# Optimization experiments

Measured on AMD Instinct MI355X. Metric: run time of the kernel, lower is better.

## Reference

```python
import math
import jax, jax.numpy as jnp
import numpy as np

B, S, D, H, DK = 2, 2048, 1024, 16, 64
NUM_BUCKETS, MAX_DISTANCE = 32, 128


def _relative_position_bucket(rel_pos):
    # bidirectional=True (encoder): is_decoder=False
    nb = NUM_BUCKETS // 2
    rel_buckets = (rel_pos > 0).astype(jnp.int32) * nb
    rp = jnp.abs(rel_pos)
    max_exact = nb // 2
    is_small = rp < max_exact
    rp_large = max_exact + (
        jnp.log(rp.astype(jnp.float32) / max_exact)
        / math.log(MAX_DISTANCE / max_exact)
        * (nb - max_exact)
    ).astype(jnp.int32)
    rp_large = jnp.minimum(rp_large, nb - 1)
    return rel_buckets + jnp.where(is_small, rp, rp_large)


def compute_bias(rel_bias, q_len, k_len):
    ctx = jnp.arange(q_len, dtype=jnp.int32)[:, None]
    mem = jnp.arange(k_len, dtype=jnp.int32)[None, :]
    buckets = _relative_position_bucket(mem - ctx)          # [q,k]
    vals = rel_bias[buckets]                                 # [q,k,H]
    return jnp.transpose(vals, (2, 0, 1))[None]              # [1,H,q,k]


def setup_inputs() -> dict:
    key = jax.random.key(0)
    ks = jax.random.split(key, 6)
    scale = 0.02
    return {
        "hidden_states": jax.random.normal(ks[0], (B, S, D), jnp.float32),
        "Wq": jax.random.normal(ks[1], (D, H * DK), jnp.float32) * scale,
        "Wk": jax.random.normal(ks[2], (D, H * DK), jnp.float32) * scale,
        "Wv": jax.random.normal(ks[3], (D, H * DK), jnp.float32) * scale,
        "Wo": jax.random.normal(ks[4], (H * DK, D), jnp.float32) * scale,
        "rel_bias": jax.random.normal(ks[5], (NUM_BUCKETS, H), jnp.float32) * scale,
    }


def reference(hidden_states, Wq, Wk, Wv, Wo, rel_bias):
    b, s, _ = hidden_states.shape

    def shape(x):  # [b,s,H*DK] -> [b,H,s,DK]
        return x.reshape(b, s, H, DK).transpose(0, 2, 1, 3)

    q = shape(hidden_states @ Wq)
    k = shape(hidden_states @ Wk)
    v = shape(hidden_states @ Wv)

    # T5: no 1/sqrt(d_k) scaling
    scores = jnp.einsum("bhqd,bhkd->bhqk", q, k)
    position_bias = compute_bias(rel_bias, s, s)             # [1,H,s,s]
    scores = scores + position_bias
    attn = jax.nn.softmax(scores.astype(jnp.float32), axis=-1).astype(scores.dtype)
    out = jnp.einsum("bhqk,bhkd->bhqd", attn, v)
    out = out.transpose(0, 2, 1, 3).reshape(b, s, H * DK)
    return out @ Wo
```

## Files before the change

kernel.cpp:

```cpp
#include <hip/hip_runtime.h>

#define HH 16
#define DKK 64
#define SS 2048
#define BB 2
#define DD 1024

typedef __attribute__((ext_vector_type(4))) float f32x4;
typedef __attribute__((ext_vector_type(16))) float f32x16;
typedef __attribute__((ext_vector_type(8))) short bf16x8;
typedef __attribute__((ext_vector_type(4))) short s16x4;
typedef __attribute__((ext_vector_type(4))) int i32x4;

#define WAITCNT_VM0 0xF70

__device__ __forceinline__ short bf16b(float f) {
    union { float f; unsigned u; } x; x.f = f;
    unsigned r = (x.u + 0x7fffu + ((x.u >> 16) & 1u)) >> 16;
    return (short)r;
}

__device__ __forceinline__ f32x4 mfma16(bf16x8 a, bf16x8 b, f32x4 c) {
    return __builtin_amdgcn_mfma_f32_16x16x32_bf16(a, b, c, 0, 0, 0);
}

__device__ __forceinline__ f32x16 mfma32(bf16x8 a, bf16x8 b, f32x16 c) {
    return __builtin_amdgcn_mfma_f32_32x32x16_bf16(a, b, c, 0, 0, 0);
}

__device__ __forceinline__ void lds16(const short* g, short* l) {
    __builtin_amdgcn_global_load_lds(
        (const __attribute__((address_space(1))) void*)g,
        (__attribute__((address_space(3))) void*)l, 16, 0, 0);
}

__device__ __forceinline__ int cvtpk(float lo, float hi) {
    int r;
    asm("v_cvt_pk_bf16_f32 %0, %1, %2" : "=v"(r) : "v"(lo), "v"(hi));
    return r;
}

__device__ __forceinline__ void swap32(int& a, int& b) {
    asm("v_permlane32_swap_b32 %0, %1" : "+v"(a), "+v"(b));
}

__global__ __launch_bounds__(256) void prep(
    const float* __restrict__ hs,
    const float* __restrict__ W0, const float* __restrict__ W1,
    const float* __restrict__ W2, const float* __restrict__ W3,
    const float* __restrict__ rb,
    short* __restrict__ hsb,
    short* __restrict__ T0, short* __restrict__ T1,
    short* __restrict__ T2, short* __restrict__ T3,
    float* __restrict__ tab) {
    __shared__ short tile[32][33];
    int blk = blockIdx.x, tid = threadIdx.x;
    if (blk < 4096) {
        int i = (blk * 256 + tid) * 4;
        f32x4 v = *(const f32x4*)(hs + i);
        s16x4 o;
        o.x = bf16b(v.x); o.y = bf16b(v.y); o.z = bf16b(v.z); o.w = bf16b(v.w);
        *(s16x4*)(hsb + i) = o;
    } else if (blk < 8192) {
        int t = blk - 4096;
        int z = t >> 10, r = t & 1023;
        int bx = r & 31, by = r >> 5;
        const float* W; short* T;
        switch (z) {
            case 0: W = W0; T = T0; break;
            case 1: W = W1; T = T1; break;
            case 2: W = W2; T = T2; break;
            default: W = W3; T = T3; break;
        }
        int n0 = bx * 32, k0 = by * 32;
        int tx = tid & 31, ty = (tid >> 5) * 4;
#pragma unroll
        for (int i = 0; i < 4; i++)
            tile[ty + i][tx] = bf16b(W[(k0 + ty + i) * DD + n0 + tx]);
        __syncthreads();
#pragma unroll
        for (int i = 0; i < 4; i++)
            T[(n0 + ty + i) * DD + k0 + tx] = tile[tx][ty + i];
    } else {
        int idx = (blk - 8192) * 256 + tid;
        if (idx < HH * 4095) {
            int h = idx / 4095, d = idx % 4095;
            int rel = d - 2047;
            int bucket = (rel > 0) ? 16 : 0;
            unsigned rr = (rel < 0) ? (unsigned)(-rel) : (unsigned)rel;
            int add;
            if (rr < 8) add = (int)rr;
            else {
                int e = 31 - __clz(rr);
                unsigned long long r2 = (unsigned long long)rr * (unsigned long long)rr;
                int f = 2 * e + ((r2 >= (2ull << (2 * e))) ? 1 : 0);
                add = 8 + (f - 6);
                if (add > 15) add = 15;
            }
            bucket += add;
            tab[h * 4095 + d] = rb[bucket * HH + h] * 1.44269504f;
        }
    }
}

__global__ __launch_bounds__(256) void gemm_qkv(
    const short* __restrict__ A, const short* __restrict__ Wt,
    short* __restrict__ Cq, short* __restrict__ Ck, short* __restrict__ Cvt) {
    const int K = 1024;
    __shared__ short As[128 * 64];
    __shared__ short Bs[128 * 64];
    int tid = threadIdx.x;
    int wave = tid >> 6, lane = tid & 63;
    int quad = lane >> 4, l16 = lane & 15;
    int m0 = blockIdx.y * 128, n0 = blockIdx.x * 128;

    int wm = (wave & 1) * 64, wn = (wave >> 1) * 64;
    int r0 = tid >> 3;
    int c0 = ((tid & 7) ^ (r0 & 7)) * 8;
    int ex7 = l16 & 7;

    f32x4 acc[4][4];
#pragma unroll
    for (int i = 0; i < 4; i++)
#pragma unroll
        for (int j = 0; j < 4; j++) acc[i][j] = (f32x4){0.f, 0.f, 0.f, 0.f};

    for (int k0 = 0; k0 < K; k0 += 64) {
        __syncthreads();
#pragma unroll
        for (int j = 0; j < 4; j++) {
            lds16(A + (size_t)(m0 + j * 32 + r0) * K + k0 + c0,
                  As + j * 2048 + wave * 512);
            lds16(Wt + (size_t)(n0 + j * 32 + r0) * K + k0 + c0,
                  Bs + j * 2048 + wave * 512);
        }
        __syncthreads();
#pragma unroll
        for (int kh = 0; kh < 2; kh++) {
            bf16x8 af[4], bfr[4];
#pragma unroll
            for (int t = 0; t < 4; t++) {
                int sl = (((kh * 4 + quad) ^ ex7)) * 8;
                af[t] = *(const bf16x8*)(As + (wm + t * 16 + l16) * 64 + sl);
                bfr[t] = *(const bf16x8*)(Bs + (wn + t * 16 + l16) * 64 + sl);
            }
#pragma unroll
            for (int mt = 0; mt < 4; mt++)
#pragma unroll
                for (int nt = 0; nt < 4; nt++)
                    acc[mt][nt] = mfma16(af[mt], bfr[nt], acc[mt][nt]);
        }
    }

#pragma unroll
    for (int mt = 0; mt < 4; mt++) {
#pragma unroll
        for (int nt = 0; nt < 4; nt++) {
#pragma unroll
            for (int r = 0; r < 4; r++) {
                int gm = m0 + wm + mt * 16 + quad * 4 + r;
                int gn = n0 + wn + nt * 16 + l16;
                int b = gm >> 11, s = gm & 2047;
                int which = gn >> 10;
                int h = (gn >> 6) & 15, dk = gn & 63;
                short bv = bf16b(acc[mt][nt][r]);
                if (which == 0)
                    Cq[(((size_t)(b * HH + h)) * SS + s) * DKK + dk] = bv;
                else if (which == 1)
                    Ck[(((size_t)(b * HH + h)) * SS + s) * DKK + dk] = bv;
                else
                    Cvt[(((size_t)(b * HH + h)) * DKK + dk) * SS + s] = bv;
            }
        }
    }
}

__global__ __launch_bounds__(256) void gemm_out(
    const short* __restrict__ A, const short* __restrict__ Wt,
    float* __restrict__ Cout) {
    const int K = 1024, N = 1024;
    __shared__ short As[64 * 64];
    __shared__ short Bs[128 * 64];
    int tid = threadIdx.x;
    int wave = tid >> 6, lane = tid & 63;
    int quad = lane >> 4, l16 = lane & 15;
    int m0 = blockIdx.y * 64, n0 = blockIdx.x * 128;

    int wm = (wave & 1) * 32, wn = (wave >> 1) * 64;
    int r0 = tid >> 3;
    int c0 = ((tid & 7) ^ (r0 & 7)) * 8;
    int ex7 = l16 & 7;

    f32x4 acc[2][4];
#pragma unroll
    for (int i = 0; i < 2; i++)
#pragma unroll
        for (int j = 0; j < 4; j++) acc[i][j] = (f32x4){0.f, 0.f, 0.f, 0.f};

    for (int k0 = 0; k0 < K; k0 += 64) {
        __syncthreads();
#pragma unroll
        for (int j = 0; j < 2; j++)
            lds16(A + (size_t)(m0 + j * 32 + r0) * K + k0 + c0,
                  As + j * 2048 + wave * 512);
#pragma unroll
        for (int j = 0; j < 4; j++)
            lds16(Wt + (size_t)(n0 + j * 32 + r0) * K + k0 + c0,
                  Bs + j * 2048 + wave * 512);
        __syncthreads();
#pragma unroll
        for (int kh = 0; kh < 2; kh++) {
            bf16x8 af[2], bfr[4];
            int sl = (((kh * 4 + quad) ^ ex7)) * 8;
#pragma unroll
            for (int t = 0; t < 2; t++)
                af[t] = *(const bf16x8*)(As + (wm + t * 16 + l16) * 64 + sl);
#pragma unroll
            for (int t = 0; t < 4; t++)
                bfr[t] = *(const bf16x8*)(Bs + (wn + t * 16 + l16) * 64 + sl);
#pragma unroll
            for (int mt = 0; mt < 2; mt++)
#pragma unroll
                for (int nt = 0; nt < 4; nt++)
                    acc[mt][nt] = mfma16(af[mt], bfr[nt], acc[mt][nt]);
        }
    }

#pragma unroll
    for (int mt = 0; mt < 2; mt++)
#pragma unroll
        for (int nt = 0; nt < 4; nt++)
#pragma unroll
            for (int r = 0; r < 4; r++) {
                int gm = m0 + wm + mt * 16 + quad * 4 + r;
                int gn = n0 + wn + nt * 16 + l16;
                Cout[(size_t)gm * N + gn] = acc[mt][nt][r];
            }
}

__global__ __launch_bounds__(256, 2) void attn(
    const short* __restrict__ Q, const short* __restrict__ Kmat,
    const short* __restrict__ Vt, const float* __restrict__ btab,
    short* __restrict__ O) {
    __shared__ short Ks[2][64 * 64];
    __shared__ short Vs[2][64 * 64];
    __shared__ float Linv[4][32];

    int tid = threadIdx.x;
    int wave = tid >> 6, lane = tid & 63;
    int el = lane & 31, hi = lane >> 5;
    int ex7 = el & 7;
    int bh = blockIdx.x;
    int h = bh & 15, b = bh >> 4;
    int q0b = blockIdx.y * 128;
    int q0w = q0b + wave * 32;

    const short* Qb = Q + (size_t)bh * SS * DKK;
    const short* Kb = Kmat + (size_t)bh * SS * DKK;
    const short* Vb = Vt + (size_t)bh * DKK * SS;
    const float* bt = btab + h * 4095;

    float blo = bt[2047 - 128];
    float bhi = bt[2047 + 128];

    int kro = tid >> 3;
    int gk = (tid & 7) ^ (kro & 7);
    const short* Kg0 = Kb + (size_t)kro * DKK + gk * 8;
    const short* Kg1 = Kb + (size_t)(kro + 32) * DKK + gk * 8;
    const short* Vg0 = Vb + (size_t)kro * SS + gk * 8;
    const short* Vg1 = Vb + (size_t)(kro + 32) * SS + gk * 8;

    bf16x8 qB[4];
#pragma unroll
    for (int c = 0; c < 4; c++)
        qB[c] = *(const bf16x8*)(Qb + (size_t)(q0w + el) * DKK + c * 16 + hi * 8);

    f32x16 o0, o1;
#pragma unroll
    for (int i = 0; i < 16; i++) { o0[i] = 0.f; o1[i] = 0.f; }
    float ls0 = 0.f, ls1 = 0.f, ls2 = 0.f, ls3 = 0.f;

    int bq = 2047 - q0w - el;

    lds16(Kg0, &Ks[0][wave * 512]);
    lds16(Kg1, &Ks[0][2048 + wave * 512]);
    lds16(Vg0, &Vs[0][wave * 512]);
    lds16(Vg1, &Vs[0][2048 + wave * 512]);

    int cur = 0;
    for (int kc = 0; kc < SS; kc += 64) {
        __syncthreads();
        int kn = (kc + 64) & (SS - 1);
        int nxt = cur ^ 1;
        lds16(Kg0 + (size_t)kn * DKK, &Ks[nxt][wave * 512]);
        lds16(Kg1 + (size_t)kn * DKK, &Ks[nxt][2048 + wave * 512]);
        lds16(Vg0 + kn, &Vs[nxt][wave * 512]);
        lds16(Vg1 + kn, &Vs[nxt][2048 + wave * 512]);

        const short* Ksc = &Ks[cur][0];
        const short* Vsc = &Vs[cur][0];

        bf16x8 vf[4][2];
#pragma unroll
        for (int c4 = 0; c4 < 4; c4++)
#pragma unroll
            for (int m = 0; m < 2; m++)
                vf[c4][m] = *(const bf16x8*)(
                    Vsc + (m * 32 + el) * 64 + (((2 * c4 + hi) ^ ex7) * 8));

#pragma unroll
        for (int st = 0; st < 2; st++) {
            f32x16 acc;
#pragma unroll
            for (int i = 0; i < 16; i++) acc[i] = 0.f;
#pragma unroll
            for (int c = 0; c < 4; c++) {
                bf16x8 kA = *(const bf16x8*)(
                    Ksc + (st * 32 + el) * 64 + (((2 * c + hi) ^ ex7) * 8));
                acc = mfma32(kA, qB[c], acc);
            }

            int ks = kc + st * 32;
            float br[16];
            if (ks > q0w - 159 && ks < q0w + 159) {
#pragma unroll
                for (int r = 0; r < 16; r++)
                    br[r] = bt[bq + ks + ((r & 3) + 8 * (r >> 2) + 4 * hi)];
            } else {
                float bc = (ks <= q0w - 159) ? blo : bhi;
#pragma unroll
                for (int r = 0; r < 16; r++) br[r] = bc;
            }

            float p[16];
#pragma unroll
            for (int r = 0; r < 16; r++)
                p[r] = __builtin_amdgcn_exp2f(
                    fmaf(acc[r], 1.44269504f, br[r]));
#pragma unroll
            for (int r = 0; r < 16; r += 4) {
                ls0 += p[r]; ls1 += p[r + 1]; ls2 += p[r + 2]; ls3 += p[r + 3];
            }

            int A1 = cvtpk(p[0], p[1]),   A2 = cvtpk(p[2], p[3]);
            int B1 = cvtpk(p[4], p[5]),   B2 = cvtpk(p[6], p[7]);
            int C1 = cvtpk(p[8], p[9]),   C2 = cvtpk(p[10], p[11]);
            int D1 = cvtpk(p[12], p[13]), D2 = cvtpk(p[14], p[15]);
            swap32(A1, B1); swap32(A2, B2);
            swap32(C1, D1); swap32(C2, D2);
            bf16x8 pf0 = __builtin_bit_cast(bf16x8, (i32x4){A1, A2, B1, B2});
            bf16x8 pf1 = __builtin_bit_cast(bf16x8, (i32x4){C1, C2, D1, D2});

            o0 = mfma32(pf0, vf[st * 2 + 0][0], o0);
            o1 = mfma32(pf0, vf[st * 2 + 0][1], o1);
            o0 = mfma32(pf1, vf[st * 2 + 1][0], o0);
            o1 = mfma32(pf1, vf[st * 2 + 1][1], o1);
        }
        cur ^= 1;
    }
    __builtin_amdgcn_s_waitcnt(WAITCNT_VM0);

    float lsum = (ls0 + ls1) + (ls2 + ls3);
    float tot = lsum + __shfl_xor(lsum, 32);
    float inv = 1.f / tot;
    if (hi == 0) Linv[wave][el] = inv;
    __asm__ __volatile__("" ::: "memory");

#pragma unroll
    for (int r = 0; r < 16; r++) {
        int qm = (r & 3) + 8 * (r >> 2) + 4 * hi;
        float iv = Linv[wave][qm];
        size_t base = ((size_t)(b * SS + q0w + qm)) * (HH * DKK) + h * DKK;
        O[base + el] = bf16b(o0[r] * iv);
        O[base + 32 + el] = bf16b(o1[r] * iv);
    }
}

extern "C" void kernel_launch(void* const* d_in, const int* in_sizes, int n_in,
                              void* d_out, int out_size, void* d_ws, size_t ws_size,
                              hipStream_t stream) {
    const float* hs = (const float*)d_in[0];
    const float* Wq = (const float*)d_in[1];
    const float* Wk = (const float*)d_in[2];
    const float* Wv = (const float*)d_in[3];
    const float* Wo = (const float*)d_in[4];
    const float* rb = (const float*)d_in[5];
    float* out = (float*)d_out;

    char* ws = (char*)d_ws;
    size_t off = 0;
    auto alloc = [&](size_t bytes) -> void* {
        void* p = (void*)(ws + off);
        off += (bytes + 255) & ~(size_t)255;
        return p;
    };
    const size_t M = (size_t)BB * SS;
    short* hsb = (short*)alloc(M * DD * 2);
    short* WqT = (short*)alloc((size_t)DD * DD * 2);
    short* WkT = (short*)alloc((size_t)DD * DD * 2);
    short* WvT = (short*)alloc((size_t)DD * DD * 2);
    short* WoT = (short*)alloc((size_t)DD * DD * 2);
    short* Qb  = (short*)alloc(M * DD * 2);
    short* Kb  = (short*)alloc(M * DD * 2);
    short* VTb = (short*)alloc(M * DD * 2);
    short* Ab  = (short*)alloc(M * DD * 2);
    float* btab = (float*)alloc((size_t)HH * 4095 * 4);

    prep<<<8448, 256, 0, stream>>>(hs, Wq, Wk, Wv, Wo, rb,
                                   hsb, WqT, WkT, WvT, WoT, btab);
    gemm_qkv<<<dim3(24, 32), 256, 0, stream>>>(hsb, WqT, Qb, Kb, VTb);
    attn<<<dim3(32, 16), 256, 0, stream>>>(Qb, Kb, VTb, btab, Ab);
    gemm_out<<<dim3(8, 64), 256, 0, stream>>>(Ab, WoT, out);
}
```

Measured before the change: 190.3 us.

## Fuse four kernels into one persistent megakernel with grid-wide barriers

Replaces the prep, QKV GEMM, attention and output GEMM launches with a single persistent kernel of 768 blocks. The phases are separated by atomic-counter grid barriers, and shared memory is unioned across phases. The aim is to remove inter-kernel launch gaps and tail effects. The costs are spin-wait barriers, only 512 of 768 blocks working in the attention and output phases, a launch bound of 3 blocks per CU that may limit registers, and reliance on every block being co-resident.

```diff
diff --git a/kernel.cpp b/kernel.cpp
--- a/kernel.cpp
+++ b/kernel.cpp
@@ -5,6 +5,7 @@
 #define SS 2048
 #define BB 2
 #define DD 1024
+#define NBLK 768
 
 typedef __attribute__((ext_vector_type(4))) float f32x4;
 typedef __attribute__((ext_vector_type(16))) float f32x16;
@@ -44,7 +45,20 @@
     asm("v_permlane32_swap_b32 %0, %1" : "+v"(a), "+v"(b));
 }
 
-__global__ __launch_bounds__(256) void prep(
+__device__ __forceinline__ void gsync(unsigned* bar, unsigned target) {
+    __syncthreads();
+    if (threadIdx.x == 0) {
+        __threadfence();
+        __hip_atomic_fetch_add(bar, 1u, __ATOMIC_ACQ_REL,
+                               __HIP_MEMORY_SCOPE_AGENT);
+        while (__hip_atomic_load(bar, __ATOMIC_ACQUIRE,
+                                 __HIP_MEMORY_SCOPE_AGENT) < target)
+            __builtin_amdgcn_s_sleep(4);
+    }
+    __syncthreads();
+}
+
+__global__ __launch_bounds__(256, 3) void mega(
     const float* __restrict__ hs,
     const float* __restrict__ W0, const float* __restrict__ W1,
     const float* __restrict__ W2, const float* __restrict__ W3,
@@ -52,327 +66,331 @@
     short* __restrict__ hsb,
     short* __restrict__ T0, short* __restrict__ T1,
     short* __restrict__ T2, short* __restrict__ T3,
-    float* __restrict__ tab) {
-    __shared__ short tile[32][33];
-    int blk = blockIdx.x, tid = threadIdx.x;
-    if (blk < 4096) {
-        int i = (blk * 256 + tid) * 4;
-        f32x4 v = *(const f32x4*)(hs + i);
-        s16x4 o;
-        o.x = bf16b(v.x); o.y = bf16b(v.y); o.z = bf16b(v.z); o.w = bf16b(v.w);
-        *(s16x4*)(hsb + i) = o;
-    } else if (blk < 8192) {
-        int t = blk - 4096;
-        int z = t >> 10, r = t & 1023;
-        int bx = r & 31, by = r >> 5;
-        const float* W; short* T;
-        switch (z) {
-            case 0: W = W0; T = T0; break;
-            case 1: W = W1; T = T1; break;
-            case 2: W = W2; T = T2; break;
-            default: W = W3; T = T3; break;
-        }
-        int n0 = bx * 32, k0 = by * 32;
-        int tx = tid & 31, ty = (tid >> 5) * 4;
+    float* __restrict__ tab,
+    short* __restrict__ Qb_, short* __restrict__ Kb_, short* __restrict__ VTb,
+    short* __restrict__ Ab, float* __restrict__ out,
+    unsigned* __restrict__ bars) {
+    __shared__ union {
+        short tile[32][33];
+        struct { short As[128 * 64]; short Bs[128 * 64]; } g;
+        struct { short Ks[2][4096]; short Vs[2][4096];
+                 float Linv[4][32]; } a;
+        struct { short As[64 * 64]; short Bs[128 * 64]; } o;
+    } sm;
+
+    int bid = blockIdx.x, tid = threadIdx.x;
+
+    for (int u = 0; u < 11; u++) {
+        int blk = bid + u * NBLK;
+        if (blk < 4096) {
+            int i = (blk * 256 + tid) * 4;
+            f32x4 v = *(const f32x4*)(hs + i);
+            s16x4 o;
+            o.x = bf16b(v.x); o.y = bf16b(v.y); o.z = bf16b(v.z); o.w = bf16b(v.w);
+            *(s16x4*)(hsb + i) = o;
+        } else if (blk < 8192) {
+            int t = blk - 4096;
+            int z = t >> 10, r = t & 1023;
+            int bx = r & 31, by = r >> 5;
+            const float* W; short* T;
+            switch (z) {
+                case 0: W = W0; T = T0; break;
+                case 1: W = W1; T = T1; break;
+                case 2: W = W2; T = T2; break;
+                default: W = W3; T = T3; break;
+            }
+            int n0 = bx * 32, k0 = by * 32;
+            int tx = tid & 31, ty = (tid >> 5) * 4;
+#pragma unroll
+            for (int i = 0; i < 4; i++)
+                sm.tile[ty + i][tx] = bf16b(W[(k0 + ty + i) * DD + n0 + tx]);
+            __syncthreads();
+#pragma unroll
+            for (int i = 0; i < 4; i++)
+                T[(n0 + ty + i) * DD + k0 + tx] = sm.tile[tx][ty + i];
+        } else {
+            int idx = (blk - 8192) * 256 + tid;
+            if (idx < HH * 4095) {
+                int h = idx / 4095, d = idx % 4095;
+                int rel = d - 2047;
+                int bucket = (rel > 0) ? 16 : 0;
+                unsigned rr = (rel < 0) ? (unsigned)(-rel) : (unsigned)rel;
+                int add;
+                if (rr < 8) add = (int)rr;
+                else {
+                    int e = 31 - __clz(rr);
+                    unsigned long long r2 =
+                        (unsigned long long)rr * (unsigned long long)rr;
+                    int f = 2 * e + ((r2 >= (2ull << (2 * e))) ? 1 : 0);
+                    add = 8 + (f - 6);
+                    if (add > 15) add = 15;
+                }
+                bucket += add;
+                tab[h * 4095 + d] = rb[bucket * HH + h] * 1.44269504f;
+            }
+        }
+        __syncthreads();
+    }
+    gsync(&bars[0], NBLK);
+
+    {
+        const int K = 1024;
+        int wave = tid >> 6, lane = tid & 63;
+        int quad = lane >> 4, l16 = lane & 15;
+        int m0 = (bid / 24) * 128, n0 = (bid % 24) * 128;
+
+        int wm = (wave & 1) * 64, wn = (wave >> 1) * 64;
+        int r0 = tid >> 3;
+        int c0 = ((tid & 7) ^ (r0 & 7)) * 8;
+        int ex7 = l16 & 7;
+
+        f32x4 acc[4][4];
 #pragma unroll
         for (int i = 0; i < 4; i++)
-            tile[ty + i][tx] = bf16b(W[(k0 + ty + i) * DD + n0 + tx]);
-        __syncthreads();
-#pragma unroll
-        for (int i = 0; i < 4; i++)
-            T[(n0 + ty + i) * DD + k0 + tx] = tile[tx][ty + i];
-    } else {
-        int idx = (blk - 8192) * 256 + tid;
-        if (idx < HH * 4095) {
-            int h = idx / 4095, d = idx % 4095;
-            int rel = d - 2047;
-            int bucket = (rel > 0) ? 16 : 0;
-            unsigned rr = (rel < 0) ? (unsigned)(-rel) : (unsigned)rel;
-            int add;
-            if (rr < 8) add = (int)rr;
-            else {
-                int e = 31 - __clz(rr);
-                unsigned long long r2 = (unsigned long long)rr * (unsigned long long)rr;
-                int f = 2 * e + ((r2 >= (2ull << (2 * e))) ? 1 : 0);
-                add = 8 + (f - 6);
-                if (add > 15) add = 15;
-            }
-            bucket += add;
-            tab[h * 4095 + d] = rb[bucket * HH + h] * 1.44269504f;
+#pragma unroll
+            for (int j = 0; j < 4; j++) acc[i][j] = (f32x4){0.f, 0.f, 0.f, 0.f};
+
+        const short* A = hsb;
+        const short* Wt = T0;
+        for (int k0 = 0; k0 < K; k0 += 64) {
+            __syncthreads();
+#pragma unroll
+            for (int j = 0; j < 4; j++) {
+                lds16(A + (size_t)(m0 + j * 32 + r0) * K + k0 + c0,
+                      sm.g.As + j * 2048 + wave * 512);
+                lds16(Wt + (size_t)(n0 + j * 32 + r0) * K + k0 + c0,
+                      sm.g.Bs + j * 2048 + wave * 512);
+            }
+            __syncthreads();
+#pragma unroll
+            for (int kh = 0; kh < 2; kh++) {
+                bf16x8 af[4], bfr[4];
+#pragma unroll
+                for (int t = 0; t < 4; t++) {
+                    int sl = (((kh * 4 + quad) ^ ex7)) * 8;
+                    af[t] = *(const bf16x8*)(sm.g.As + (wm + t * 16 + l16) * 64 + sl);
+                    bfr[t] = *(const bf16x8*)(sm.g.Bs + (wn + t * 16 + l16) * 64 + sl);
+                }
+#pragma unroll
+                for (int mt = 0; mt < 4; mt++)
+#pragma unroll
+                    for (int nt = 0; nt < 4; nt++)
+                        acc[mt][nt] = mfma16(af[mt], bfr[nt], acc[mt][nt]);
+            }
+        }
+
+#pragma unroll
+        for (int mt = 0; mt < 4; mt++) {
+#pragma unroll
+            for (int nt = 0; nt < 4; nt++) {
+#pragma unroll
+                for (int r = 0; r < 4; r++) {
+                    int gm = m0 + wm + mt * 16 + quad * 4 + r;
+                    int gn = n0 + wn + nt * 16 + l16;
+                    int b = gm >> 11, s = gm & 2047;
+                    int which = gn >> 10;
+                    int h = (gn >> 6) & 15, dk = gn & 63;
+                    short bv = bf16b(acc[mt][nt][r]);
+                    if (which == 0)
+                        Qb_[(((size_t)(b * HH + h)) * SS + s) * DKK + dk] = bv;
+                    else if (which == 1)
+                        Kb_[(((size_t)(b * HH + h)) * SS + s) * DKK + dk] = bv;
+                    else
+                        VTb[(((size_t)(b * HH + h)) * DKK + dk) * SS + s] = bv;
+                }
+            }
         }
     }
-}
-
-__global__ __launch_bounds__(256) void gemm_qkv(
-    const short* __restrict__ A, const short* __restrict__ Wt,
-    short* __restrict__ Cq, short* __restrict__ Ck, short* __restrict__ Cvt) {
-    const int K = 1024;
-    __shared__ short As[128 * 64];
-    __shared__ short Bs[128 * 64];
-    int tid = threadIdx.x;
-    int wave = tid >> 6, lane = tid & 63;
-    int quad = lane >> 4, l16 = lane & 15;
-    int m0 = blockIdx.y * 128, n0 = blockIdx.x * 128;
-
-    int wm = (wave & 1) * 64, wn = (wave >> 1) * 64;
-    int r0 = tid >> 3;
-    int c0 = ((tid & 7) ^ (r0 & 7)) * 8;
-    int ex7 = l16 & 7;
-
-    f32x4 acc[4][4];
-#pragma unroll
-    for (int i = 0; i < 4; i++)
-#pragma unroll
-        for (int j = 0; j < 4; j++) acc[i][j] = (f32x4){0.f, 0.f, 0.f, 0.f};
-
-    for (int k0 = 0; k0 < K; k0 += 64) {
-        __syncthreads();
-#pragma unroll
-        for (int j = 0; j < 4; j++) {
-            lds16(A + (size_t)(m0 + j * 32 + r0) * K + k0 + c0,
-                  As + j * 2048 + wave * 512);
-            lds16(Wt + (size_t)(n0 + j * 32 + r0) * K + k0 + c0,
-                  Bs + j * 2048 + wave * 512);
-        }
-        __syncthreads();
-#pragma unroll
-        for (int kh = 0; kh < 2; kh++) {
-            bf16x8 af[4], bfr[4];
-#pragma unroll
-            for (int t = 0; t < 4; t++) {
+    gsync(&bars[16], NBLK);
+
+    if (bid < 512) {
+        int wave = tid >> 6, lane = tid & 63;
+        int el = lane & 31, hi = lane >> 5;
+        int ex7 = el & 7;
+        int bh = bid & 31;
+        int h = bh & 15, b = bh >> 4;
+        int q0b = (bid >> 5) * 128;
+        int q0w = q0b + wave * 32;
+
+        const short* Qp = Qb_ + (size_t)bh * SS * DKK;
+        const short* Kp = Kb_ + (size_t)bh * SS * DKK;
+        const short* Vp = VTb + (size_t)bh * DKK * SS;
+        const float* bt = tab + h * 4095;
+
+        float blo = bt[2047 - 128];
+        float bhi = bt[2047 + 128];
+
+        int kro = tid >> 3;
+        int gk = (tid & 7) ^ (kro & 7);
+        const short* Kg0 = Kp + (size_t)kro * DKK + gk * 8;
+        const short* Kg1 = Kp + (size_t)(kro + 32) * DKK + gk * 8;
+        const short* Vg0 = Vp + (size_t)kro * SS + gk * 8;
+        const short* Vg1 = Vp + (size_t)(kro + 32) * SS + gk * 8;
+
+        bf16x8 qB[4];
+#pragma unroll
+        for (int c = 0; c < 4; c++)
+            qB[c] = *(const bf16x8*)(Qp + (size_t)(q0w + el) * DKK + c * 16 + hi * 8);
+
+        f32x16 o0, o1;
+#pragma unroll
+        for (int i = 0; i < 16; i++) { o0[i] = 0.f; o1[i] = 0.f; }
+        float ls0 = 0.f, ls1 = 0.f, ls2 = 0.f, ls3 = 0.f;
+
+        int bq = 2047 - q0w - el;
+
+        lds16(Kg0, &sm.a.Ks[0][wave * 512]);
+        lds16(Kg1, &sm.a.Ks[0][2048 + wave * 512]);
+        lds16(Vg0, &sm.a.Vs[0][wave * 512]);
+        lds16(Vg1, &sm.a.Vs[0][2048 + wave * 512]);
+
+        int cur = 0;
+        for (int kc = 0; kc < SS; kc += 64) {
+            __syncthreads();
+            int kn = (kc + 64) & (SS - 1);
+            int nxt = cur ^ 1;
+            lds16(Kg0 + (size_t)kn * DKK, &sm.a.Ks[nxt][wave * 512]);
+            lds16(Kg1 + (size_t)kn * DKK, &sm.a.Ks[nxt][2048 + wave * 512]);
+            lds16(Vg0 + kn, &sm.a.Vs[nxt][wave * 512]);
+            lds16(Vg1 + kn, &sm.a.Vs[nxt][2048 + wave * 512]);
+
+            const short* Ksc = &sm.a.Ks[cur][0];
+            const short* Vsc = &sm.a.Vs[cur][0];
+
+            bf16x8 vf[4][2];
+#pragma unroll
+            for (int c4 = 0; c4 < 4; c4++)
+#pragma unroll
+                for (int m = 0; m < 2; m++)
+                    vf[c4][m] = *(const bf16x8*)(
+                        Vsc + (m * 32 + el) * 64 + (((2 * c4 + hi) ^ ex7) * 8));
+
+#pragma unroll
+            for (int st = 0; st < 2; st++) {
+                f32x16 acc;
+#pragma unroll
+                for (int i = 0; i < 16; i++) acc[i] = 0.f;
+#pragma unroll
+                for (int c = 0; c < 4; c++) {
+                    bf16x8 kA = *(const bf16x8*)(
+                        Ksc + (st * 32 + el) * 64 + (((2 * c + hi) ^ ex7) * 8));
+                    acc = mfma32(kA, qB[c], acc);
+                }
+
+                int ks = kc + st * 32;
+                float br[16];
+                if (ks > q0w - 159 && ks < q0w + 159) {
+#pragma unroll
+                    for (int r = 0; r < 16; r++)
+                        br[r] = bt[bq + ks + ((r & 3) + 8 * (r >> 2) + 4 * hi)];
+                } else {
+                    float bc = (ks <= q0w - 159) ? blo : bhi;
+#pragma unroll
+                    for (int r = 0; r < 16; r++) br[r] = bc;
+                }
+
+                float p[16];
+#pragma unroll
+                for (int r = 0; r < 16; r++)
+                    p[r] = __builtin_amdgcn_exp2f(
+                        fmaf(acc[r], 1.44269504f, br[r]));
+#pragma unroll
+                for (int r = 0; r < 16; r += 4) {
+                    ls0 += p[r]; ls1 += p[r + 1]; ls2 += p[r + 2]; ls3 += p[r + 3];
+                }
+
+                int A1 = cvtpk(p[0], p[1]),   A2 = cvtpk(p[2], p[3]);
+                int B1 = cvtpk(p[4], p[5]),   B2 = cvtpk(p[6], p[7]);
+                int C1 = cvtpk(p[8], p[9]),   C2 = cvtpk(p[10], p[11]);
+                int D1 = cvtpk(p[12], p[13]), D2 = cvtpk(p[14], p[15]);
+                swap32(A1, B1); swap32(A2, B2);
+                swap32(C1, D1); swap32(C2, D2);
+                bf16x8 pf0 = __builtin_bit_cast(bf16x8, (i32x4){A1, A2, B1, B2});
+                bf16x8 pf1 = __builtin_bit_cast(bf16x8, (i32x4){C1, C2, D1, D2});
+
+                o0 = mfma32(pf0, vf[st * 2 + 0][0], o0);
+                o1 = mfma32(pf0, vf[st * 2 + 0][1], o1);
+                o0 = mfma32(pf1, vf[st * 2 + 1][0], o0);
+                o1 = mfma32(pf1, vf[st * 2 + 1][1], o1);
+            }
+            cur ^= 1;
+        }
+        __builtin_amdgcn_s_waitcnt(WAITCNT_VM0);
+
+        float lsum = (ls0 + ls1) + (ls2 + ls3);
+        float tot = lsum + __shfl_xor(lsum, 32);
+        float inv = 1.f / tot;
+        if (hi == 0) sm.a.Linv[wave][el] = inv;
+        __asm__ __volatile__("" ::: "memory");
+
+#pragma unroll
+        for (int r = 0; r < 16; r++) {
+            int qm = (r & 3) + 8 * (r >> 2) + 4 * hi;
+            float iv = sm.a.Linv[wave][qm];
+            size_t base = ((size_t)(b * SS + q0w + qm)) * (HH * DKK) + h * DKK;
+            Ab[base + el] = bf16b(o0[r] * iv);
+            Ab[base + 32 + el] = bf16b(o1[r] * iv);
+        }
+    }
+    gsync(&bars[32], NBLK);
+
+    if (bid < 512) {
+        const int K = 1024, N = 1024;
+        int wave = tid >> 6, lane = tid & 63;
+        int quad = lane >> 4, l16 = lane & 15;
+        int m0 = (bid >> 3) * 64, n0 = (bid & 7) * 128;
+
+        int wm = (wave & 1) * 32, wn = (wave >> 1) * 64;
+        int r0 = tid >> 3;
+        int c0 = ((tid & 7) ^ (r0 & 7)) * 8;
+        int ex7 = l16 & 15 & 7;
+
+        f32x4 acc[2][4];
+#pragma unroll
+        for (int i = 0; i < 2; i++)
+#pragma unroll
+            for (int j = 0; j < 4; j++) acc[i][j] = (f32x4){0.f, 0.f, 0.f, 0.f};
+
+        const short* Wt = T3;
+        for (int k0 = 0; k0 < K; k0 += 64) {
+            __syncthreads();
+#pragma unroll
+            for (int j = 0; j < 2; j++)
+                lds16(Ab + (size_t)(m0 + j * 32 + r0) * K + k0 + c0,
+                      sm.o.As + j * 2048 + wave * 512);
+#pragma unroll
+            for (int j = 0; j < 4; j++)
+                lds16(Wt + (size_t)(n0 + j * 32 + r0) * K + k0 + c0,
+                      sm.o.Bs + j * 2048 + wave * 512);
+            __syncthreads();
+#pragma unroll
+            for (int kh = 0; kh < 2; kh++) {
+                bf16x8 af[2], bfr[4];
                 int sl = (((kh * 4 + quad) ^ ex7)) * 8;
-                af[t] = *(const bf16x8*)(As + (wm + t * 16 + l16) * 64 + sl);
-                bfr[t] = *(const bf16x8*)(Bs + (wn + t * 16 + l16) * 64 + sl);
-            }
-#pragma unroll
-            for (int mt = 0; mt < 4; mt++)
-#pragma unroll
-                for (int nt = 0; nt < 4; nt++)
-                    acc[mt][nt] = mfma16(af[mt], bfr[nt], acc[mt][nt]);
-        }
-    }
-
-#pragma unroll
-    for (int mt = 0; mt < 4; mt++) {
-#pragma unroll
-        for (int nt = 0; nt < 4; nt++) {
-#pragma unroll
-            for (int r = 0; r < 4; r++) {
-                int gm = m0 + wm + mt * 16 + quad * 4 + r;
-                int gn = n0 + wn + nt * 16 + l16;
-                int b = gm >> 11, s = gm & 2047;
-                int which = gn >> 10;
-                int h = (gn >> 6) & 15, dk = gn & 63;
-                short bv = bf16b(acc[mt][nt][r]);
-                if (which == 0)
-                    Cq[(((size_t)(b * HH + h)) * SS + s) * DKK + dk] = bv;
-                else if (which == 1)
-                    Ck[(((size_t)(b * HH + h)) * SS + s) * DKK + dk] = bv;
-                else
-                    Cvt[(((size_t)(b * HH + h)) * DKK + dk) * SS + s] = bv;
-            }
-        }
-    }
-}
-
-__global__ __launch_bounds__(256) void gemm_out(
-    const short* __restrict__ A, const short* __restrict__ Wt,
-    float* __restrict__ Cout) {
-    const int K = 1024, N = 1024;
-    __shared__ short As[64 * 64];
-    __shared__ short Bs[128 * 64];
-    int tid = threadIdx.x;
-    int wave = tid >> 6, lane = tid & 63;
-    int quad = lane >> 4, l16 = lane & 15;
-    int m0 = blockIdx.y * 64, n0 = blockIdx.x * 128;
-
-    int wm = (wave & 1) * 32, wn = (wave >> 1) * 64;
-    int r0 = tid >> 3;
-    int c0 = ((tid & 7) ^ (r0 & 7)) * 8;
-    int ex7 = l16 & 7;
-
-    f32x4 acc[2][4];
-#pragma unroll
-    for (int i = 0; i < 2; i++)
-#pragma unroll
-        for (int j = 0; j < 4; j++) acc[i][j] = (f32x4){0.f, 0.f, 0.f, 0.f};
-
-    for (int k0 = 0; k0 < K; k0 += 64) {
-        __syncthreads();
-#pragma unroll
-        for (int j = 0; j < 2; j++)
-            lds16(A + (size_t)(m0 + j * 32 + r0) * K + k0 + c0,
-                  As + j * 2048 + wave * 512);
-#pragma unroll
-        for (int j = 0; j < 4; j++)
-            lds16(Wt + (size_t)(n0 + j * 32 + r0) * K + k0 + c0,
-                  Bs + j * 2048 + wave * 512);
-        __syncthreads();
-#pragma unroll
-        for (int kh = 0; kh < 2; kh++) {
-            bf16x8 af[2], bfr[4];
-            int sl = (((kh * 4 + quad) ^ ex7)) * 8;
-#pragma unroll
-            for (int t = 0; t < 2; t++)
-                af[t] = *(const bf16x8*)(As + (wm + t * 16 + l16) * 64 + sl);
-#pragma unroll
-            for (int t = 0; t < 4; t++)
-                bfr[t] = *(const bf16x8*)(Bs + (wn + t * 16 + l16) * 64 + sl);
-#pragma unroll
-            for (int mt = 0; mt < 2; mt++)
-#pragma unroll
-                for (int nt = 0; nt < 4; nt++)
-                    acc[mt][nt] = mfma16(af[mt], bfr[nt], acc[mt][nt]);
-        }
-    }
-
-#pragma unroll
-    for (int mt = 0; mt < 2; mt++)
-#pragma unroll
-        for (int nt = 0; nt < 4; nt++)
-#pragma unroll
-            for (int r = 0; r < 4; r++) {
-                int gm = m0 + wm + mt * 16 + quad * 4 + r;
-                int gn = n0 + wn + nt * 16 + l16;
-                Cout[(size_t)gm * N + gn] = acc[mt][nt][r];
-            }
-}
-
-__global__ __launch_bounds__(256, 2) void attn(
-    const short* __restrict__ Q, const short* __restrict__ Kmat,
-    const short* __restrict__ Vt, const float* __restrict__ btab,
-    short* __restrict__ O) {
-    __shared__ short Ks[2][64 * 64];
-    __shared__ short Vs[2][64 * 64];
-    __shared__ float Linv[4][32];
-
-    int tid = threadIdx.x;
-    int wave = tid >> 6, lane = tid & 63;
-    int el = lane & 31, hi = lane >> 5;
-    int ex7 = el & 7;
-    int bh = blockIdx.x;
-    int h = bh & 15, b = bh >> 4;
-    int q0b = blockIdx.y * 128;
-    int q0w = q0b + wave * 32;
-
-    const short* Qb = Q + (size_t)bh * SS * DKK;
-    const short* Kb = Kmat + (size_t)bh * SS * DKK;
-    const short* Vb = Vt + (size_t)bh * DKK * SS;
-    const float* bt = btab + h * 4095;
-
-    float blo = bt[2047 - 128];
-    float bhi = bt[2047 + 128];
-
-    int kro = tid >> 3;
-    int gk = (tid & 7) ^ (kro & 7);
-    const short* Kg0 = Kb + (size_t)kro * DKK + gk * 8;
-    const short* Kg1 = Kb + (size_t)(kro + 32) * DKK + gk * 8;
-    const short* Vg0 = Vb + (size_t)kro * SS + gk * 8;
-    const short* Vg1 = Vb + (size_t)(kro + 32) * SS + gk * 8;
-
-    bf16x8 qB[4];
-#pragma unroll
-    for (int c = 0; c < 4; c++)
-        qB[c] = *(const bf16x8*)(Qb + (size_t)(q0w + el) * DKK + c * 16 + hi * 8);
-
-    f32x16 o0, o1;
-#pragma unroll
-    for (int i = 0; i < 16; i++) { o0[i] = 0.f; o1[i] = 0.f; }
-    float ls0 = 0.f, ls1 = 0.f, ls2 = 0.f, ls3 = 0.f;
-
-    int bq = 2047 - q0w - el;
-
-    lds16(Kg0, &Ks[0][wave * 512]);
-    lds16(Kg1, &Ks[0][2048 + wave * 512]);
-    lds16(Vg0, &Vs[0][wave * 512]);
-    lds16(Vg1, &Vs[0][2048 + wave * 512]);
-
-    int cur = 0;
-    for (int kc = 0; kc < SS; kc += 64) {
-        __syncthreads();
-        int kn = (kc + 64) & (SS - 1);
-        int nxt = cur ^ 1;
-        lds16(Kg0 + (size_t)kn * DKK, &Ks[nxt][wave * 512]);
-        lds16(Kg1 + (size_t)kn * DKK, &Ks[nxt][2048 + wave * 512]);
-        lds16(Vg0 + kn, &Vs[nxt][wave * 512]);
-        lds16(Vg1 + kn, &Vs[nxt][2048 + wave * 512]);
-
-        const short* Ksc = &Ks[cur][0];
-        const short* Vsc = &Vs[cur][0];
-
-        bf16x8 vf[4][2];
-#pragma unroll
-        for (int c4 = 0; c4 < 4; c4++)
-#pragma unroll
-            for (int m = 0; m < 2; m++)
-                vf[c4][m] = *(const bf16x8*)(
-                    Vsc + (m * 32 + el) * 64 + (((2 * c4 + hi) ^ ex7) * 8));
-
-#pragma unroll
-        for (int st = 0; st < 2; st++) {
-            f32x16 acc;
-#pragma unroll
-            for (int i = 0; i < 16; i++) acc[i] = 0.f;
-#pragma unroll
-            for (int c = 0; c < 4; c++) {
-                bf16x8 kA = *(const bf16x8*)(
-                    Ksc + (st * 32 + el) * 64 + (((2 * c + hi) ^ ex7) * 8));
-                acc = mfma32(kA, qB[c], acc);
-            }
-
-            int ks = kc + st * 32;
-            float br[16];
-            if (ks > q0w - 159 && ks < q0w + 159) {
-#pragma unroll
-                for (int r = 0; r < 16; r++)
-                    br[r] = bt[bq + ks + ((r & 3) + 8 * (r >> 2) + 4 * hi)];
-            } else {
-                float bc = (ks <= q0w - 159) ? blo : bhi;
-#pragma unroll
-                for (int r = 0; r < 16; r++) br[r] = bc;
-            }
-
-            float p[16];
-#pragma unroll
-            for (int r = 0; r < 16; r++)
-                p[r] = __builtin_amdgcn_exp2f(
-                    fmaf(acc[r], 1.44269504f, br[r]));
-#pragma unroll
-            for (int r = 0; r < 16; r += 4) {
-                ls0 += p[r]; ls1 += p[r + 1]; ls2 += p[r + 2]; ls3 += p[r + 3];
-            }
-
-            int A1 = cvtpk(p[0], p[1]),   A2 = cvtpk(p[2], p[3]);
-            int B1 = cvtpk(p[4], p[5]),   B2 = cvtpk(p[6], p[7]);
-            int C1 = cvtpk(p[8], p[9]),   C2 = cvtpk(p[10], p[11]);
-            int D1 = cvtpk(p[12], p[13]), D2 = cvtpk(p[14], p[15]);
-            swap32(A1, B1); swap32(A2, B2);
-            swap32(C1, D1); swap32(C2, D2);
-            bf16x8 pf0 = __builtin_bit_cast(bf16x8, (i32x4){A1, A2, B1, B2});
-            bf16x8 pf1 = __builtin_bit_cast(bf16x8, (i32x4){C1, C2, D1, D2});
-
-            o0 = mfma32(pf0, vf[st * 2 + 0][0], o0);
-            o1 = mfma32(pf0, vf[st * 2 + 0][1], o1);
-            o0 = mfma32(pf1, vf[st * 2 + 1][0], o0);
-            o1 = mfma32(pf1, vf[st * 2 + 1][1], o1);
-        }
-        cur ^= 1;
-    }
-    __builtin_amdgcn_s_waitcnt(WAITCNT_VM0);
-
-    float lsum = (ls0 + ls1) + (ls2 + ls3);
-    float tot = lsum + __shfl_xor(lsum, 32);
-    float inv = 1.f / tot;
-    if (hi == 0) Linv[wave][el] = inv;
-    __asm__ __volatile__("" ::: "memory");
-
-#pragma unroll
-    for (int r = 0; r < 16; r++) {
-        int qm = (r & 3) + 8 * (r >> 2) + 4 * hi;
-        float iv = Linv[wave][qm];
-        size_t base = ((size_t)(b * SS + q0w + qm)) * (HH * DKK) + h * DKK;
-        O[base + el] = bf16b(o0[r] * iv);
-        O[base + 32 + el] = bf16b(o1[r] * iv);
+#pragma unroll
+                for (int t = 0; t < 2; t++)
+                    af[t] = *(const bf16x8*)(sm.o.As + (wm + t * 16 + l16) * 64 + sl);
+#pragma unroll
+                for (int t = 0; t < 4; t++)
+                    bfr[t] = *(const bf16x8*)(sm.o.Bs + (wn + t * 16 + l16) * 64 + sl);
+#pragma unroll
+                for (int mt = 0; mt < 2; mt++)
+#pragma unroll
+                    for (int nt = 0; nt < 4; nt++)
+                        acc[mt][nt] = mfma16(af[mt], bfr[nt], acc[mt][nt]);
+            }
+        }
+
+#pragma unroll
+        for (int mt = 0; mt < 2; mt++)
+#pragma unroll
+            for (int nt = 0; nt < 4; nt++)
+#pragma unroll
+                for (int r = 0; r < 4; r++) {
+                    int gm = m0 + wm + mt * 16 + quad * 4 + r;
+                    int gn = n0 + wn + nt * 16 + l16;
+                    out[(size_t)gm * N + gn] = acc[mt][nt][r];
+                }
     }
 }
 
@@ -405,10 +423,10 @@
     short* VTb = (short*)alloc(M * DD * 2);
     short* Ab  = (short*)alloc(M * DD * 2);
     float* btab = (float*)alloc((size_t)HH * 4095 * 4);
-
-    prep<<<8448, 256, 0, stream>>>(hs, Wq, Wk, Wv, Wo, rb,
-                                   hsb, WqT, WkT, WvT, WoT, btab);
-    gemm_qkv<<<dim3(24, 32), 256, 0, stream>>>(hsb, WqT, Qb, Kb, VTb);
-    attn<<<dim3(32, 16), 256, 0, stream>>>(Qb, Kb, VTb, btab, Ab);
-    gemm_out<<<dim3(8, 64), 256, 0, stream>>>(Ab, WoT, out);
-}
+    unsigned* bars = (unsigned*)alloc(256);
+
+    hipMemsetAsync(bars, 0, 256, stream);
+    mega<<<NBLK, 256, 0, stream>>>(hs, Wq, Wk, Wv, Wo, rb,
+                                   hsb, WqT, WkT, WvT, WoT, btab,
+                                   Qb, Kb, VTb, Ab, out, bars);
+}
```

Measured after the change: 652.4 us. 3.43x slower.
